# Optimization experiments

Hardware: AMD Instinct MI355X
Metric: run time of the kernel (lower is better)

## Reference

```python
import jax, jax.numpy as jnp
import numpy as np

V = 32000   # vocab_size
E = 200     # embedding_size
H = 256     # LSTM hidden size (hard-coded in module)
B = 16      # batch
T = 256     # seq_len


def setup_inputs() -> dict:
    key = jax.random.key(0)
    ks = jax.random.split(key, 12)

    def init(k, shape, scale):
        return jax.random.normal(k, shape, jnp.float32) * scale

    inp = {"x": jax.random.randint(ks[0], (B, T), 0, V)}
    inp["emb"] = init(ks[1], (V, E), 0.02)
    dims = [E, H, H]
    s = 1.0 / float(np.sqrt(H))
    for l in range(3):
        inp[f"Wi{l}"] = init(ks[2 + 3 * l], (4 * H, dims[l]), s)  # input weights (gate order i,f,g,o)
        inp[f"Wh{l}"] = init(ks[3 + 3 * l], (4 * H, H), s)        # recurrent weights
        inp[f"b{l}"] = jnp.zeros((4 * H,), jnp.float32)
    inp["fcW"] = init(ks[11], (V, H), s)
    inp["fcb"] = jnp.zeros((V,), jnp.float32)
    return inp


def _lstm_layer(x, Wi, Wh, b):
    # x: [B, T, C_in] -> [B, T, H]; standard LSTM, zero initial state.
    xg = jnp.einsum('btc,gc->btg', x, Wi) + b  # precompute input projections [B,T,4H]
    Hh = Wh.shape[1]

    def step(carry, xt):
        h, c = carry
        g = xt + h @ Wh.T                      # [B, 4H]
        i, f, gg, o = jnp.split(g, 4, axis=-1)
        i = jax.nn.sigmoid(i)
        f = jax.nn.sigmoid(f)
        gg = jnp.tanh(gg)
        o = jax.nn.sigmoid(o)
        c = f * c + i * gg
        h = o * jnp.tanh(c)
        return (h, c), h

    h0 = jnp.zeros((x.shape[0], Hh), x.dtype)
    _, hs = jax.lax.scan(step, (h0, h0), jnp.swapaxes(xg, 0, 1))  # time-major scan
    return jnp.swapaxes(hs, 0, 1)


def reference(x, emb, Wi0, Wh0, b0, Wi1, Wh1, b1, Wi2, Wh2, b2, fcW, fcb):
    out = emb[x]  # [B, T, E]
    for Wi, Wh, b in ((Wi0, Wh0, b0), (Wi1, Wh1, b1), (Wi2, Wh2, b2)):
        out = _lstm_layer(out, Wi, Wh, b)
    logits = out @ fcW.T + fcb  # [B, T, V]
    return jax.nn.log_softmax(logits, axis=-1)
```

## Files before the change

kernel.cpp:

```cpp
#include <hip/hip_runtime.h>
#include <stdint.h>

typedef __attribute__((ext_vector_type(8))) short bf16x8;
typedef __attribute__((ext_vector_type(4))) float f32x4;

#define DEV __device__ __forceinline__

DEV unsigned short f2bf(float f) {
    unsigned b = __float_as_uint(f);
    unsigned r = (b + 0x7fffu + ((b >> 16) & 1u)) >> 16;
    return (unsigned short)r;
}
DEV unsigned pack2(float a, float b) {
    return (unsigned)f2bf(a) | ((unsigned)f2bf(b) << 16);
}
DEV bf16x8 pack8(float4 f0, float4 f1) {
    bf16x8 r;
    r[0] = (short)f2bf(f0.x); r[1] = (short)f2bf(f0.y);
    r[2] = (short)f2bf(f0.z); r[3] = (short)f2bf(f0.w);
    r[4] = (short)f2bf(f1.x); r[5] = (short)f2bf(f1.y);
    r[6] = (short)f2bf(f1.z); r[7] = (short)f2bf(f1.w);
    return r;
}
DEV float sigm(float x) { return 1.f / (1.f + __expf(-x)); }
DEV float tanh_f(float x) {
    float t = __expf(-2.f * fabsf(x));
    float r = (1.f - t) / (1.f + t);
    return copysignf(r, x);
}
DEV int ldsw(int row, int cb) { return row * 512 + (cb ^ ((row & 7) << 4)); }

#define OFF_HB0   65536
#define OFF_HB1   (65536 + 4194304)
#define OFF_XEA   (65536 + 8388608)
#define OFF_HS    (OFF_XEA + 2097152)
#define OFF_WB    (OFF_HS + 2097152)
#define WB_BYTES  (32000u * 256u * 2u)

__global__ __launch_bounds__(256) void k_embed(const int* __restrict__ x,
                                               const float* __restrict__ emb,
                                               unsigned short* __restrict__ XeA)
{
    int row = blockIdx.x * 8 + (threadIdx.x >> 5);
    int i = threadIdx.x & 31;
    int tok = x[row];
    int b = row >> 8, t = row & 255;
    uint4 v = make_uint4(0, 0, 0, 0);
    if (i < 25) {
        const float* p = emb + (size_t)tok * 200 + i * 8;
        float4 f0 = *(const float4*)p;
        float4 f1 = *(const float4*)(p + 4);
        v.x = pack2(f0.x, f0.y); v.y = pack2(f0.z, f0.w);
        v.z = pack2(f1.x, f1.y); v.w = pack2(f1.z, f1.w);
    }
    int kt = i >> 2, qq = i & 3;
    *(uint4*)(XeA + (size_t)t * 4096 + (size_t)((kt * 64 + qq * 16 + b) * 8)) = v;
}

__global__ __launch_bounds__(256) void k_wcvt(const float* __restrict__ W,
                                              unsigned short* __restrict__ Wb)
{
    size_t i = ((size_t)blockIdx.x * 256 + threadIdx.x) * 8;
    float4 f0 = *(const float4*)(W + i);
    float4 f1 = *(const float4*)(W + i + 4);
    uint4 v;
    v.x = pack2(f0.x, f0.y); v.y = pack2(f0.z, f0.w);
    v.z = pack2(f1.x, f1.y); v.w = pack2(f1.z, f1.w);
    *(uint4*)(Wb + i) = v;
}

template <int WB>
__global__ __launch_bounds__(256) void k_fcbig(const unsigned short* __restrict__ X,
                                               const float* __restrict__ W,
                                               const unsigned short* __restrict__ Wb,
                                               const float* __restrict__ bias,
                                               float* __restrict__ outf)
{
    __shared__ __align__(16) char Abuf[65536];
    __shared__ __align__(16) char Bbuf[65536];
    const int tid = threadIdx.x, lane = tid & 63, wave = tid >> 6;
    const int wm = wave >> 1, wn = wave & 1;
    const int bn = blockIdx.x, bm = blockIdx.y;
    const int l15 = lane & 15, q = lane >> 4;

#pragma unroll
    for (int it = 0; it < 16; ++it) {
        int p = tid + it * 256;
        int row = p >> 5, c8 = p & 31;
        uint4 bv;
        if (WB) {
            bv = *(const uint4*)(Wb + (size_t)(bn * 128 + row) * 256 + c8 * 8);
        } else {
            const float* wp = W + (size_t)(bn * 128 + row) * 256 + c8 * 8;
            float4 f0 = *(const float4*)wp;
            float4 f1 = *(const float4*)(wp + 4);
            bv.x = pack2(f0.x, f0.y); bv.y = pack2(f0.z, f0.w);
            bv.z = pack2(f1.x, f1.y); bv.w = pack2(f1.z, f1.w);
        }
        *(uint4*)(Bbuf + ldsw(row, c8 * 16)) = bv;
    }

    float bvv[4];
#pragma unroll
    for (int nt = 0; nt < 4; ++nt) bvv[nt] = bias[bn * 128 + wn * 64 + nt * 16 + l15];

    for (int ms = 0; ms < 8; ++ms) {
        __syncthreads();
#pragma unroll
        for (int it = 0; it < 16; ++it) {
            int p = tid + it * 256;
            int row = p >> 5, c8 = p & 31;
            uint4 av = *(const uint4*)(X + (size_t)(bm * 1024 + ms * 128 + row) * 256 + c8 * 8);
            *(uint4*)(Abuf + ldsw(row, c8 * 16)) = av;
        }
        __syncthreads();

        f32x4 acc[4][4];
#pragma unroll
        for (int a = 0; a < 4; a++)
#pragma unroll
            for (int b = 0; b < 4; b++) acc[a][b] = f32x4{0.f, 0.f, 0.f, 0.f};

#pragma unroll
        for (int kt = 0; kt < 8; ++kt) {
            bf16x8 a[4], b[4];
#pragma unroll
            for (int mt = 0; mt < 4; ++mt)
                a[mt] = *(const bf16x8*)(Abuf + ldsw(wm * 64 + mt * 16 + l15, kt * 64 + q * 16));
#pragma unroll
            for (int nt = 0; nt < 4; ++nt)
                b[nt] = *(const bf16x8*)(Bbuf + ldsw(wn * 64 + nt * 16 + l15, kt * 64 + q * 16));
#pragma unroll
            for (int mt = 0; mt < 4; ++mt)
#pragma unroll
                for (int nt = 0; nt < 4; ++nt)
                    acc[mt][nt] = __builtin_amdgcn_mfma_f32_16x16x32_bf16(a[mt], b[nt], acc[mt][nt], 0, 0, 0);
        }

#pragma unroll
        for (int nt = 0; nt < 4; ++nt) {
            int gn = bn * 128 + wn * 64 + nt * 16 + l15;
#pragma unroll
            for (int mt = 0; mt < 4; ++mt) {
#pragma unroll
                for (int r = 0; r < 4; ++r) {
                    int gm = bm * 1024 + ms * 128 + wm * 64 + mt * 16 + q * 4 + r;
                    outf[(size_t)gm * 32000 + gn] = acc[mt][nt][r] + bvv[nt];
                }
            }
        }
    }
}

__global__ __launch_bounds__(1024) void k_lsesub(float* __restrict__ lg)
{
    __shared__ float sm[16], ss[16];
    __shared__ float sL;
    const int row = blockIdx.x, tid = threadIdx.x;
    float* p = lg + (size_t)row * 32000;
    float4 v0[4], v1[4];
    float m = -3.0e38f, s = 0.f;
#pragma unroll
    for (int k = 0; k < 4; ++k) {
        int g = tid + (k << 10);
        if (g < 4000) {
            v0[k] = *(const float4*)(p + g * 8);
            v1[k] = *(const float4*)(p + g * 8 + 4);
            float a0 = fmaxf(fmaxf(v0[k].x, v0[k].y), fmaxf(v0[k].z, v0[k].w));
            float a1 = fmaxf(fmaxf(v1[k].x, v1[k].y), fmaxf(v1[k].z, v1[k].w));
            float ml = fmaxf(a0, a1);
            if (ml > m) { s *= __expf(m - ml); m = ml; }
            s += __expf(v0[k].x - m) + __expf(v0[k].y - m) + __expf(v0[k].z - m) + __expf(v0[k].w - m)
               + __expf(v1[k].x - m) + __expf(v1[k].y - m) + __expf(v1[k].z - m) + __expf(v1[k].w - m);
        }
    }
#pragma unroll
    for (int off = 32; off; off >>= 1) {
        float m2 = __shfl_xor(m, off);
        float s2 = __shfl_xor(s, off);
        float nm = fmaxf(m, m2);
        s = s * __expf(m - nm) + s2 * __expf(m2 - nm);
        m = nm;
    }
    if ((tid & 63) == 0) { sm[tid >> 6] = m; ss[tid >> 6] = s; }
    __syncthreads();
    if (tid == 0) {
        float M = sm[0], S = ss[0];
        for (int w = 1; w < 16; ++w) {
            float m2 = sm[w], s2 = ss[w];
            float nm = fmaxf(M, m2);
            S = S * __expf(M - nm) + s2 * __expf(m2 - nm);
            M = nm;
        }
        sL = M + __logf(S);
    }
    __syncthreads();
    const float L = sL;
#pragma unroll
    for (int k = 0; k < 4; ++k) {
        int g = tid + (k << 10);
        if (g < 4000) {
            v0[k].x -= L; v0[k].y -= L; v0[k].z -= L; v0[k].w -= L;
            v1[k].x -= L; v1[k].y -= L; v1[k].z -= L; v1[k].w -= L;
            *(float4*)(p + g * 8) = v0[k];
            *(float4*)(p + g * 8 + 4) = v1[k];
        }
    }
}

__global__ __launch_bounds__(256) void k_scan3(
    const float* __restrict__ Wi0, const float* __restrict__ Wh0, const float* __restrict__ b0,
    const float* __restrict__ Wi1, const float* __restrict__ Wh1, const float* __restrict__ b1,
    const float* __restrict__ Wi2, const float* __restrict__ Wh2, const float* __restrict__ b2,
    const unsigned short* __restrict__ XeA,
    unsigned short* __restrict__ hseq,
    unsigned long long* __restrict__ Hb0,
    unsigned long long* __restrict__ Hb1,
    unsigned long long* __restrict__ ring2)
{
    __shared__ __align__(16) unsigned short hX[4096];
    __shared__ __align__(16) unsigned short hH[4096];
    __shared__ float gbuf[64 * 17];
    const int tid = threadIdx.x, lane = tid & 63, wave = tid >> 6;
    const int L = blockIdx.x >> 4, s = blockIdx.x & 15;
    const int l15 = lane & 15, q = lane >> 4;
    const int grow = wave * 256 + s * 16 + l15;

    const float* Wi = (L == 0) ? Wi0 : ((L == 1) ? Wi1 : Wi2);
    const float* Wh = (L == 0) ? Wh0 : ((L == 1) ? Wh1 : Wh2);
    const float* bb = (L == 0) ? b0 : ((L == 1) ? b1 : b2);
    const int KX = (L == 0) ? 200 : 256;

    bf16x8 WiR[8], WhR[8];
#pragma unroll
    for (int kt = 0; kt < 8; ++kt) {
        int k0 = kt * 32 + q * 8;
        {
            const float* p = Wh + (size_t)grow * 256 + k0;
            WhR[kt] = pack8(*(const float4*)p, *(const float4*)(p + 4));
        }
        if (k0 < KX) {
            const float* p = Wi + (size_t)grow * KX + k0;
            WiR[kt] = pack8(*(const float4*)p, *(const float4*)(p + 4));
        } else {
            WiR[kt] = bf16x8{0, 0, 0, 0, 0, 0, 0, 0};
        }
    }
    const float bv = bb[grow];

    const int eb = tid >> 4, eu = tid & 15;
    const bool pub = (eu & 1) == 0;
    int slot;
    {
        int ug = s * 16 + eu;
        int kt = ug >> 5, qq = (ug >> 3) & 3, j = ug & 7;
        slot = ((kt * 64 + qq * 16 + eb) * 8 + j) >> 1;
    }
    float c = 0.f;
    unsigned* hX32 = (unsigned*)hX;
    unsigned* hH32 = (unsigned*)hH;

    const unsigned long long* xbase = (L == 1) ? Hb0 : Hb1;
    unsigned long long* obase = (L == 0) ? Hb0 : Hb1;
    const unsigned long long* rbase = (L == 0) ? Hb0 : Hb1;

    for (int t = 0; t < 256; ++t) {
        if (L == 0) {
            const unsigned* srcx = (const unsigned*)(XeA + (size_t)t * 4096);
            *(uint4*)(hX32 + tid * 8)     = *(const uint4*)(srcx + tid * 8);
            *(uint4*)(hX32 + tid * 8 + 4) = *(const uint4*)(srcx + tid * 8 + 4);
        }
        {
            unsigned long long vx[8], vh[8];
            unsigned pendx = (L > 0) ? 0xffu : 0u;
            unsigned pendh = (t > 0) ? 0xffu : 0u;
            const unsigned long long* sx = xbase + (size_t)t * 2048 + tid;
            const unsigned long long* sh =
                (L == 2) ? (ring2 + ((t - 1) & 1) * 2048 + tid)
                         : (rbase + (size_t)((t > 0) ? (t - 1) : 0) * 2048 + tid);
            const unsigned ex = (unsigned)(t + 1), eh = (unsigned)t;
            while (pendx | pendh) {
#pragma unroll
                for (int i = 0; i < 8; ++i)
                    if (pendx & (1u << i))
                        vx[i] = __hip_atomic_load(sx + i * 256, __ATOMIC_RELAXED,
                                                  __HIP_MEMORY_SCOPE_AGENT);
#pragma unroll
                for (int i = 0; i < 8; ++i)
                    if (pendh & (1u << i))
                        vh[i] = __hip_atomic_load(sh + i * 256, __ATOMIC_RELAXED,
                                                  __HIP_MEMORY_SCOPE_AGENT);
#pragma unroll
                for (int i = 0; i < 8; ++i) {
                    if ((pendx & (1u << i)) && (unsigned)(vx[i] >> 32) == ex) pendx &= ~(1u << i);
                    if ((pendh & (1u << i)) && (unsigned)(vh[i] >> 32) == eh) pendh &= ~(1u << i);
                }
                if (pendx | pendh) __builtin_amdgcn_s_sleep(1);
            }
            if (L > 0) {
#pragma unroll
                for (int i = 0; i < 8; ++i) hX32[tid + i * 256] = (unsigned)vx[i];
            }
            if (t > 0) {
#pragma unroll
                for (int i = 0; i < 8; ++i) hH32[tid + i * 256] = (unsigned)vh[i];
            } else {
#pragma unroll
                for (int i = 0; i < 8; ++i) hH32[tid + i * 256] = 0u;
            }
        }
        __syncthreads();

        f32x4 acc0 = {bv, bv, bv, bv};
        f32x4 acc1 = {0.f, 0.f, 0.f, 0.f};
#pragma unroll
        for (int kt = 0; kt < 8; ++kt) {
            bf16x8 ax = *(const bf16x8*)(hX + (kt * 64 + lane) * 8);
            acc0 = __builtin_amdgcn_mfma_f32_16x16x32_bf16(ax, WiR[kt], acc0, 0, 0, 0);
            bf16x8 ah = *(const bf16x8*)(hH + (kt * 64 + lane) * 8);
            acc1 = __builtin_amdgcn_mfma_f32_16x16x32_bf16(ah, WhR[kt], acc1, 0, 0, 0);
        }
        {
            int rowb = wave * 16 + l15;
#pragma unroll
            for (int r = 0; r < 4; ++r) gbuf[rowb * 17 + q * 4 + r] = acc0[r] + acc1[r];
        }
        __syncthreads();

        float gi = gbuf[(0 * 16 + eu) * 17 + eb];
        float gf = gbuf[(1 * 16 + eu) * 17 + eb];
        float gg = gbuf[(2 * 16 + eu) * 17 + eb];
        float go = gbuf[(3 * 16 + eu) * 17 + eb];
        float i_ = sigm(gi), f_ = sigm(gf), g_ = tanh_f(gg), o_ = sigm(go);
        c = f_ * c + i_ * g_;
        float h = o_ * tanh_f(c);
        float hn = __shfl_xor(h, 1);
        if (pub) {
            unsigned pk = pack2(h, hn);
            unsigned long long val =
                ((unsigned long long)(unsigned)(t + 1) << 32) | (unsigned long long)pk;
            if (L == 2) {
                __hip_atomic_store(ring2 + (t & 1) * 2048 + slot, val, __ATOMIC_RELAXED,
                                   __HIP_MEMORY_SCOPE_AGENT);
                *(unsigned*)(hseq + (size_t)(eb * 256 + t) * 256 + s * 16 + eu) = pk;
            } else {
                __hip_atomic_store(obase + (size_t)t * 2048 + slot, val, __ATOMIC_RELAXED,
                                   __HIP_MEMORY_SCOPE_AGENT);
            }
        }
    }
}

extern "C" void kernel_launch(void* const* d_in, const int* in_sizes, int n_in,
                              void* d_out, int out_size, void* d_ws, size_t ws_size,
                              hipStream_t stream)
{
    const int* x = (const int*)d_in[0];
    const float* emb = (const float*)d_in[1];
    const float* Wi0 = (const float*)d_in[2];
    const float* Wh0 = (const float*)d_in[3];
    const float* b0  = (const float*)d_in[4];
    const float* Wi1 = (const float*)d_in[5];
    const float* Wh1 = (const float*)d_in[6];
    const float* b1  = (const float*)d_in[7];
    const float* Wi2 = (const float*)d_in[8];
    const float* Wh2 = (const float*)d_in[9];
    const float* b2  = (const float*)d_in[10];
    const float* fcW = (const float*)d_in[11];
    const float* fcb = (const float*)d_in[12];
    float* out = (float*)d_out;

    uint8_t* w = (uint8_t*)d_ws;
    unsigned long long* ring2 = (unsigned long long*)w;
    unsigned long long* Hb0 = (unsigned long long*)(w + OFF_HB0);
    unsigned long long* Hb1 = (unsigned long long*)(w + OFF_HB1);
    unsigned short* XeA = (unsigned short*)(w + OFF_XEA);
    unsigned short* hs  = (unsigned short*)(w + OFF_HS);
    unsigned short* Wb  = (unsigned short*)(w + OFF_WB);
    const bool wb_ok = ws_size >= (size_t)OFF_WB + (size_t)WB_BYTES;

    hipMemsetAsync(w, 0, OFF_XEA, stream);

    if (wb_ok) k_wcvt<<<4000, 256, 0, stream>>>(fcW, Wb);

    k_embed<<<512, 256, 0, stream>>>(x, emb, XeA);

    k_scan3<<<48, 256, 0, stream>>>(Wi0, Wh0, b0, Wi1, Wh1, b1, Wi2, Wh2, b2,
                                    XeA, hs, Hb0, Hb1, ring2);

    if (wb_ok)
        k_fcbig<1><<<dim3(250, 4), 256, 0, stream>>>(hs, nullptr, Wb, fcb, out);
    else
        k_fcbig<0><<<dim3(250, 4), 256, 0, stream>>>(hs, fcW, nullptr, fcb, out);

    k_lsesub<<<4096, 1024, 0, stream>>>(out);
}
```

Measured before the change: 1.448 ms.

## Load recurrent operands directly into registers per wave, dropping LDS staging

Each wave now polls and loads the full h and x operand vectors it needs straight from global memory into MFMA operand registers, instead of the block cooperatively staging them in LDS and then syncing. This removes the LDS round trip and the pre-MFMA barrier, and it skips the recurrent MFMAs at t=0. A barrier is added after the gbuf reads so the buffer is not overwritten early. In exchange every wave issues four times as many global atomic loads for the same data, and each wave spins on its own, which adds memory traffic while polling.

```diff
diff --git a/kernel.cpp b/kernel.cpp
--- a/kernel.cpp
+++ b/kernel.cpp
@@ -3,6 +3,7 @@
 
 typedef __attribute__((ext_vector_type(8))) short bf16x8;
 typedef __attribute__((ext_vector_type(4))) float f32x4;
+typedef __attribute__((ext_vector_type(4))) unsigned int u32x4;
 
 #define DEV __device__ __forceinline__
 
@@ -21,6 +22,12 @@
     r[4] = (short)f2bf(f1.x); r[5] = (short)f2bf(f1.y);
     r[6] = (short)f2bf(f1.z); r[7] = (short)f2bf(f1.w);
     return r;
+}
+DEV bf16x8 mk8(unsigned long long a, unsigned long long b,
+               unsigned long long c, unsigned long long d) {
+    union { u32x4 u; bf16x8 v; } cv;
+    cv.u = u32x4{(unsigned)a, (unsigned)b, (unsigned)c, (unsigned)d};
+    return cv.v;
 }
 DEV float sigm(float x) { return 1.f / (1.f + __expf(-x)); }
 DEV float tanh_f(float x) {
@@ -218,8 +225,6 @@
     unsigned long long* __restrict__ Hb1,
     unsigned long long* __restrict__ ring2)
 {
-    __shared__ __align__(16) unsigned short hX[4096];
-    __shared__ __align__(16) unsigned short hH[4096];
     __shared__ float gbuf[64 * 17];
     const int tid = threadIdx.x, lane = tid & 63, wave = tid >> 6;
     const int L = blockIdx.x >> 4, s = blockIdx.x & 15;
@@ -257,68 +262,89 @@
         slot = ((kt * 64 + qq * 16 + eb) * 8 + j) >> 1;
     }
     float c = 0.f;
-    unsigned* hX32 = (unsigned*)hX;
-    unsigned* hH32 = (unsigned*)hH;
 
     const unsigned long long* xbase = (L == 1) ? Hb0 : Hb1;
     unsigned long long* obase = (L == 0) ? Hb0 : Hb1;
     const unsigned long long* rbase = (L == 0) ? Hb0 : Hb1;
 
     for (int t = 0; t < 256; ++t) {
+        bf16x8 ax[8], ah[8];
+        const bool needh = (t > 0);
+        const unsigned long long* sh =
+            (L == 2) ? (ring2 + ((t - 1) & 1) * 2048 + lane * 4)
+                     : (rbase + (size_t)(needh ? (t - 1) : 0) * 2048 + lane * 4);
+        const unsigned eh = (unsigned)t;
+
         if (L == 0) {
-            const unsigned* srcx = (const unsigned*)(XeA + (size_t)t * 4096);
-            *(uint4*)(hX32 + tid * 8)     = *(const uint4*)(srcx + tid * 8);
-            *(uint4*)(hX32 + tid * 8 + 4) = *(const uint4*)(srcx + tid * 8 + 4);
-        }
-        {
-            unsigned long long vx[8], vh[8];
-            unsigned pendx = (L > 0) ? 0xffu : 0u;
-            unsigned pendh = (t > 0) ? 0xffu : 0u;
-            const unsigned long long* sx = xbase + (size_t)t * 2048 + tid;
-            const unsigned long long* sh =
-                (L == 2) ? (ring2 + ((t - 1) & 1) * 2048 + tid)
-                         : (rbase + (size_t)((t > 0) ? (t - 1) : 0) * 2048 + tid);
-            const unsigned ex = (unsigned)(t + 1), eh = (unsigned)t;
-            while (pendx | pendh) {
-#pragma unroll
-                for (int i = 0; i < 8; ++i)
-                    if (pendx & (1u << i))
-                        vx[i] = __hip_atomic_load(sx + i * 256, __ATOMIC_RELAXED,
-                                                  __HIP_MEMORY_SCOPE_AGENT);
-#pragma unroll
-                for (int i = 0; i < 8; ++i)
-                    if (pendh & (1u << i))
-                        vh[i] = __hip_atomic_load(sh + i * 256, __ATOMIC_RELAXED,
-                                                  __HIP_MEMORY_SCOPE_AGENT);
-#pragma unroll
-                for (int i = 0; i < 8; ++i) {
-                    if ((pendx & (1u << i)) && (unsigned)(vx[i] >> 32) == ex) pendx &= ~(1u << i);
-                    if ((pendh & (1u << i)) && (unsigned)(vh[i] >> 32) == eh) pendh &= ~(1u << i);
+            const unsigned short* xp = XeA + (size_t)t * 4096;
+#pragma unroll
+            for (int kt = 0; kt < 8; ++kt)
+                ax[kt] = *(const bf16x8*)(xp + (kt * 64 + lane) * 8);
+            if (needh) {
+                unsigned long long vh[8][4];
+                while (true) {
+                    bool ok = true;
+#pragma unroll
+                    for (int kt = 0; kt < 8; ++kt)
+#pragma unroll
+                        for (int j = 0; j < 4; ++j) {
+                            vh[kt][j] = __hip_atomic_load(sh + kt * 256 + j, __ATOMIC_RELAXED,
+                                                          __HIP_MEMORY_SCOPE_AGENT);
+                            ok &= ((unsigned)(vh[kt][j] >> 32) == eh);
+                        }
+                    if (ok) break;
+                    __builtin_amdgcn_s_sleep(1);
                 }
-                if (pendx | pendh) __builtin_amdgcn_s_sleep(1);
+#pragma unroll
+                for (int kt = 0; kt < 8; ++kt)
+                    ah[kt] = mk8(vh[kt][0], vh[kt][1], vh[kt][2], vh[kt][3]);
             }
-            if (L > 0) {
-#pragma unroll
-                for (int i = 0; i < 8; ++i) hX32[tid + i * 256] = (unsigned)vx[i];
+        } else {
+            const unsigned long long* sx = xbase + (size_t)t * 2048 + lane * 4;
+            const unsigned ex = (unsigned)(t + 1);
+            unsigned long long vx[8][4], vh[8][4];
+            while (true) {
+                bool ok = true;
+#pragma unroll
+                for (int kt = 0; kt < 8; ++kt)
+#pragma unroll
+                    for (int j = 0; j < 4; ++j) {
+                        vx[kt][j] = __hip_atomic_load(sx + kt * 256 + j, __ATOMIC_RELAXED,
+                                                      __HIP_MEMORY_SCOPE_AGENT);
+                        ok &= ((unsigned)(vx[kt][j] >> 32) == ex);
+                    }
+                if (needh) {
+#pragma unroll
+                    for (int kt = 0; kt < 8; ++kt)
+#pragma unroll
+                        for (int j = 0; j < 4; ++j) {
+                            vh[kt][j] = __hip_atomic_load(sh + kt * 256 + j, __ATOMIC_RELAXED,
+                                                          __HIP_MEMORY_SCOPE_AGENT);
+                            ok &= ((unsigned)(vh[kt][j] >> 32) == eh);
+                        }
+                }
+                if (ok) break;
+                __builtin_amdgcn_s_sleep(1);
             }
-            if (t > 0) {
-#pragma unroll
-                for (int i = 0; i < 8; ++i) hH32[tid + i * 256] = (unsigned)vh[i];
-            } else {
-#pragma unroll
-                for (int i = 0; i < 8; ++i) hH32[tid + i * 256] = 0u;
+#pragma unroll
+            for (int kt = 0; kt < 8; ++kt)
+                ax[kt] = mk8(vx[kt][0], vx[kt][1], vx[kt][2], vx[kt][3]);
+            if (needh) {
+#pragma unroll
+                for (int kt = 0; kt < 8; ++kt)
+                    ah[kt] = mk8(vh[kt][0], vh[kt][1], vh[kt][2], vh[kt][3]);
             }
         }
-        __syncthreads();
 
         f32x4 acc0 = {bv, bv, bv, bv};
+#pragma unroll
+        for (int kt = 0; kt < 8; ++kt)
+            acc0 = __builtin_amdgcn_mfma_f32_16x16x32_bf16(ax[kt], WiR[kt], acc0, 0, 0, 0);
         f32x4 acc1 = {0.f, 0.f, 0.f, 0.f};
-#pragma unroll
-        for (int kt = 0; kt < 8; ++kt) {
-            bf16x8 ax = *(const bf16x8*)(hX + (kt * 64 + lane) * 8);
-            acc0 = __builtin_amdgcn_mfma_f32_16x16x32_bf16(ax, WiR[kt], acc0, 0, 0, 0);
-            bf16x8 ah = *(const bf16x8*)(hH + (kt * 64 + lane) * 8);
-            acc1 = __builtin_amdgcn_mfma_f32_16x16x32_bf16(ah, WhR[kt], acc1, 0, 0, 0);
+        if (needh) {
+#pragma unroll
+            for (int kt = 0; kt < 8; ++kt)
+                acc1 = __builtin_amdgcn_mfma_f32_16x16x32_bf16(ah[kt], WhR[kt], acc1, 0, 0, 0);
         }
         {
             int rowb = wave * 16 + l15;
@@ -331,6 +357,8 @@
         float gf = gbuf[(1 * 16 + eu) * 17 + eb];
         float gg = gbuf[(2 * 16 + eu) * 17 + eb];
         float go = gbuf[(3 * 16 + eu) * 17 + eb];
+        __syncthreads();
+
         float i_ = sigm(gi), f_ = sigm(gf), g_ = tanh_f(gg), o_ = sigm(go);
         c = f_ * c + i_ * g_;
         float h = o_ * tanh_f(c);
```

Result: slower. 1.822 ms (+25.9%).
